# Optimization experiments

Measured on AMD Instinct MI355X. Metric: run time of the kernel, lower is better.

## Reference

```python
import jax, jax.numpy as jnp
import numpy as np

NQ = 4  # qubits
NL = 2  # layers actually used by the circuit body
BATCH = 1048576

def _c64(a):
    return a.astype(jnp.complex64)

def _ry(t):
    # RY(t) = [[cos(t/2), -sin(t/2)], [sin(t/2), cos(t/2)]]; t scalar or [B]
    c, s = jnp.cos(t / 2), jnp.sin(t / 2)
    return _c64(jnp.stack([jnp.stack([c, -s], -1), jnp.stack([s, c], -1)], -2))

def _rx(t):
    # RX(t) = [[cos(t/2), -i sin(t/2)], [-i sin(t/2), cos(t/2)]]
    c, s = _c64(jnp.cos(t / 2)), _c64(jnp.sin(t / 2))
    return jnp.stack([jnp.stack([c, -1j * s], -1), jnp.stack([-1j * s, c], -1)], -2)

def _rz(t):
    # RZ(t) = diag(exp(-i t/2), exp(i t/2))
    ph = _c64(t / 2)
    em, ep = jnp.exp(-1j * ph), jnp.exp(1j * ph)
    z = jnp.zeros_like(em)
    return jnp.stack([jnp.stack([em, z], -1), jnp.stack([z, ep], -1)], -2)

def _apply1q(state, gate, wire):
    # state: [B, 2,2,2,2]; gate: [2,2] (shared) or [B,2,2] (per-sample angle)
    s = jnp.moveaxis(state, wire + 1, -1)
    if gate.ndim == 3:
        out = jnp.einsum('b...j,bij->b...i', s, gate)
    else:
        out = jnp.einsum('b...j,ij->b...i', s, gate)
    return jnp.moveaxis(out, -1, wire + 1)

def _cnot(state, c, t):
    # bring control to axis 1, target to axis 2; flip target where control==1
    s = jnp.moveaxis(state, (c + 1, t + 1), (1, 2))
    s = jnp.stack([s[:, 0], jnp.flip(s[:, 1], axis=1)], axis=1)
    return jnp.moveaxis(s, (1, 2), (c + 1, t + 1))

def _circuit(x, weights):
    B = x.shape[0]
    state = jnp.zeros((B, 2 ** NQ), jnp.complex64).at[:, 0].set(1.0)
    state = state.reshape((B,) + (2,) * NQ)
    # angle encoding: RY(x_i) on wire i (per-sample angles)
    for i in range(NQ):
        state = _apply1q(state, _ry(x[:, i]), i)
    w = weights.reshape(NL, NQ, 3)
    for layer in range(NL):
        for i in range(NQ):
            state = _apply1q(state, _rx(w[layer, i, 0]), i)
            state = _apply1q(state, _ry(w[layer, i, 1]), i)
            state = _apply1q(state, _rz(w[layer, i, 2]), i)
        for i in range(NQ - 1):
            state = _cnot(state, i, i + 1)
        state = _cnot(state, NQ - 1, 0)
    # expval PauliZ on wire 0: +|amp|^2 for q0=0, -|amp|^2 for q0=1
    p = state.real ** 2 + state.imag ** 2
    p = p.reshape(B, 2, -1).sum(-1)
    return (p[:, 0] - p[:, 1]).astype(jnp.float32)

def setup_inputs() -> dict:
    key = jax.random.key(0)
    k1, k2 = jax.random.split(key)
    x = jax.random.normal(k1, (BATCH, NQ), jnp.float32)
    weights = jax.random.normal(k2, (NL * NQ * 3,), jnp.float32)
    return {"x": x, "weights": weights}

def reference(x, weights):
    return _circuit(x, weights)
```

## Files before the change

### kernel.cpp

```cpp
#include <hip/hip_runtime.h>
#include <hip/hip_bf16.h>


#define BLOCK 256
#define VEC 4

__global__ __launch_bounds__(BLOCK) void qnn_fused_kernel(
    const float4* __restrict__ x, const float* __restrict__ w,
    float* __restrict__ out, int n) {

    __shared__ float Ur[16][17], Ui[16][17];
    __shared__ float Msh[256];
    __shared__ float Ks[81];

    const int t = threadIdx.x;

    {
        const int j = t >> 4;
        const int k = t & 15;
        float ur = (k == j) ? 1.0f : 0.0f;
        float ui = 0.0f;

        #pragma unroll
        for (int layer = 0; layer < 2; ++layer) {
            #pragma unroll
            for (int q = 0; q < 4; ++q) {
                const int bit = 3 - q;
                const int str = 1 << bit;
                const int kb = (k >> bit) & 1;
                float c, s, pr, pi, nr, ni;
                __sincosf(w[(layer * 4 + q) * 3 + 0] * 0.5f, &s, &c);
                pr = __shfl_xor(ur, str);
                pi = __shfl_xor(ui, str);
                nr = c * ur + s * pi;
                ni = c * ui - s * pr;
                ur = nr; ui = ni;
                __sincosf(w[(layer * 4 + q) * 3 + 1] * 0.5f, &s, &c);
                pr = __shfl_xor(ur, str);
                pi = __shfl_xor(ui, str);
                {
                    const float sg = kb ? s : -s;
                    nr = c * ur + sg * pr;
                    ni = c * ui + sg * pi;
                }
                ur = nr; ui = ni;
                __sincosf(w[(layer * 4 + q) * 3 + 2] * 0.5f, &s, &c);
                {
                    const float sz = kb ? s : -s;
                    nr = c * ur - sz * ui;
                    ni = c * ui + sz * ur;
                }
                ur = nr; ui = ni;
            }
            #pragma unroll
            for (int g = 0; g < 4; ++g) {
                const int cw = g;
                const int tw = (g + 1) & 3;
                const int bc = 3 - cw, bt = 3 - tw;
                const float pr = __shfl_xor(ur, 1 << bt);
                const float pi = __shfl_xor(ui, 1 << bt);
                const bool ctl = (k >> bc) & 1;
                ur = ctl ? pr : ur;
                ui = ctl ? pi : ui;
            }
        }
        Ur[k][j] = ur;
        Ui[k][j] = ui;
    }
    __syncthreads();

    {
        const int a = t >> 4, b = t & 15;
        float acc = 0.0f;
        #pragma unroll
        for (int kk = 0; kk < 16; ++kk) {
            const float v2 = Ur[kk][a] * Ur[kk][b] + Ui[kk][a] * Ui[kk][b];
            acc += (kk & 8) ? -v2 : v2;
        }
        Msh[t] = acc;
    }
    __syncthreads();

    if (t < 81) {
        const int d0 = t / 27, d1 = (t / 9) % 3, d2 = (t / 3) % 3, d3 = t % 3;
        const int gd[4] = {d3, d2, d1, d0};
        float sum = 0.0f;
        #pragma unroll
        for (int m = 0; m < 16; ++m) {
            int a2 = 0, b2 = 0;
            float sign = 1.0f;
            #pragma unroll
            for (int p = 0; p < 4; ++p) {
                const int cp = (m >> p) & 1;
                if (gd[p] == 2) { a2 |= cp << p; b2 |= (1 - cp) << p; }
                else {
                    a2 |= cp << p; b2 |= cp << p;
                    if (gd[p] == 1 && cp) sign = -sign;
                }
            }
            sum += sign * Msh[a2 * 16 + b2];
        }
        Ks[t] = sum * 0.0625f;
    }
    __syncthreads();

    const int gid = blockIdx.x * BLOCK + t;
    const int stride = gridDim.x * BLOCK;

    for (int i0 = gid; i0 < n; i0 += stride * VEC) {
        int idx[VEC];
        bool ok[VEC];
        float4 xv[VEC];
        #pragma unroll
        for (int v = 0; v < VEC; ++v) {
            const int ii = i0 + v * stride;
            ok[v] = ii < n;
            idx[v] = ok[v] ? ii : (n - 1);
            xv[v] = x[idx[v]];
        }

        float C[VEC][4], S[VEC][4];
        #pragma unroll
        for (int v = 0; v < VEC; ++v) {
            __sincosf(xv[v].x, &S[v][0], &C[v][0]);
            __sincosf(xv[v].y, &S[v][1], &C[v][1]);
            __sincosf(xv[v].z, &S[v][2], &C[v][2]);
            __sincosf(xv[v].w, &S[v][3], &C[v][3]);
        }

        float r[VEC];
        #pragma unroll
        for (int d0 = 0; d0 < 3; ++d0) {
            float a1[VEC];
            #pragma unroll
            for (int d1 = 0; d1 < 3; ++d1) {
                float a2[VEC];
                #pragma unroll
                for (int d2 = 0; d2 < 3; ++d2) {
                    const int base = ((d0 * 3 + d1) * 3 + d2) * 3;
                    const float k0 = Ks[base], k1 = Ks[base + 1], k2 = Ks[base + 2];
                    #pragma unroll
                    for (int v = 0; v < VEC; ++v) {
                        const float tt = fmaf(k2, S[v][3], fmaf(k1, C[v][3], k0));
                        if (d2 == 0) a2[v] = tt;
                        else a2[v] = fmaf(tt, (d2 == 1) ? C[v][2] : S[v][2], a2[v]);
                    }
                }
                #pragma unroll
                for (int v = 0; v < VEC; ++v) {
                    if (d1 == 0) a1[v] = a2[v];
                    else a1[v] = fmaf(a2[v], (d1 == 1) ? C[v][1] : S[v][1], a1[v]);
                }
            }
            #pragma unroll
            for (int v = 0; v < VEC; ++v) {
                if (d0 == 0) r[v] = a1[v];
                else r[v] = fmaf(a1[v], (d0 == 1) ? C[v][0] : S[v][0], r[v]);
            }
        }

        #pragma unroll
        for (int v = 0; v < VEC; ++v)
            if (ok[v]) out[idx[v]] = r[v];
    }
}

extern "C" void kernel_launch(void* const* d_in, const int* in_sizes, int n_in,
                              void* d_out, int out_size, void* d_ws, size_t ws_size,
                              hipStream_t stream) {
    const float* x = (const float*)d_in[0];
    const float* w = (const float*)d_in[1];
    float* out = (float*)d_out;

    const int n = in_sizes[0] / 4;

    int grid = (n + BLOCK * VEC - 1) / (BLOCK * VEC);
    if (grid < 1) grid = 1;
    if (grid > 4096) grid = 4096;

    qnn_fused_kernel<<<grid, BLOCK, 0, stream>>>((const float4*)x, w, out, n);
}
```

Baseline: 69.87 us.

## Prefetch inputs before matrix setup, use hardware sin/cos, vectorize coefficient loads

Issues the first batch of x loads before the per-block unitary and coefficient precomputation, so global memory latency overlaps that setup work. Later iterations are software-pipelined by loading the next chunk before computing the current one. __sincosf is replaced with the raw amdgcn sin/cos instructions on angles pre-scaled by 1/(2π), which skips range reduction and may lose accuracy for large inputs. The 81 coefficients are padded into float4 slots so each LDS read fetches three coefficients at once.

Result: no change. 70.28 us (+0.6%).

```diff
diff --git a/kernel.cpp b/kernel.cpp
--- a/kernel.cpp
+++ b/kernel.cpp
@@ -4,6 +4,7 @@
 
 #define BLOCK 256
 #define VEC 4
+#define INV_2PI 0.15915494309189535f
 
 __global__ __launch_bounds__(BLOCK) void qnn_fused_kernel(
     const float4* __restrict__ x, const float* __restrict__ w,
@@ -11,9 +12,20 @@
 
     __shared__ float Ur[16][17], Ui[16][17];
     __shared__ float Msh[256];
-    __shared__ float Ks[81];
+    __shared__ float4 Ks4[27];
 
     const int t = threadIdx.x;
+    const int gid = blockIdx.x * BLOCK + t;
+    const int stride = gridDim.x * BLOCK;
+    const int step = stride * VEC;
+
+    int i0 = gid;
+    float4 xv[VEC];
+    #pragma unroll
+    for (int v = 0; v < VEC; ++v) {
+        const int ii = i0 + v * stride;
+        xv[v] = x[(ii < n) ? ii : (n > 0 ? n - 1 : 0)];
+    }
 
     {
         const int j = t >> 4;
@@ -100,32 +112,33 @@
             }
             sum += sign * Msh[a2 * 16 + b2];
         }
-        Ks[t] = sum * 0.0625f;
+        ((float*)Ks4)[(t / 3) * 4 + (t % 3)] = sum * 0.0625f;
     }
     __syncthreads();
 
-    const int gid = blockIdx.x * BLOCK + t;
-    const int stride = gridDim.x * BLOCK;
-
-    for (int i0 = gid; i0 < n; i0 += stride * VEC) {
-        int idx[VEC];
-        bool ok[VEC];
-        float4 xv[VEC];
+    for (; i0 < n;) {
+        float C[VEC][4], S[VEC][4];
         #pragma unroll
         for (int v = 0; v < VEC; ++v) {
-            const int ii = i0 + v * stride;
-            ok[v] = ii < n;
-            idx[v] = ok[v] ? ii : (n - 1);
-            xv[v] = x[idx[v]];
-        }
-
-        float C[VEC][4], S[VEC][4];
-        #pragma unroll
-        for (int v = 0; v < VEC; ++v) {
-            __sincosf(xv[v].x, &S[v][0], &C[v][0]);
-            __sincosf(xv[v].y, &S[v][1], &C[v][1]);
-            __sincosf(xv[v].z, &S[v][2], &C[v][2]);
-            __sincosf(xv[v].w, &S[v][3], &C[v][3]);
+            const float r0 = xv[v].x * INV_2PI;
+            const float r1 = xv[v].y * INV_2PI;
+            const float r2 = xv[v].z * INV_2PI;
+            const float r3 = xv[v].w * INV_2PI;
+            S[v][0] = __builtin_amdgcn_sinf(r0); C[v][0] = __builtin_amdgcn_cosf(r0);
+            S[v][1] = __builtin_amdgcn_sinf(r1); C[v][1] = __builtin_amdgcn_cosf(r1);
+            S[v][2] = __builtin_amdgcn_sinf(r2); C[v][2] = __builtin_amdgcn_cosf(r2);
+            S[v][3] = __builtin_amdgcn_sinf(r3); C[v][3] = __builtin_amdgcn_cosf(r3);
+        }
+
+        const int inext = i0 + step;
+        const bool more = inext < n;
+        float4 xn[VEC];
+        if (more) {
+            #pragma unroll
+            for (int v = 0; v < VEC; ++v) {
+                const int ii = inext + v * stride;
+                xn[v] = x[(ii < n) ? ii : (n - 1)];
+            }
         }
 
         float r[VEC];
@@ -137,11 +150,10 @@
                 float a2[VEC];
                 #pragma unroll
                 for (int d2 = 0; d2 < 3; ++d2) {
-                    const int base = ((d0 * 3 + d1) * 3 + d2) * 3;
-                    const float k0 = Ks[base], k1 = Ks[base + 1], k2 = Ks[base + 2];
+                    const float4 kf = Ks4[(d0 * 3 + d1) * 3 + d2];
                     #pragma unroll
                     for (int v = 0; v < VEC; ++v) {
-                        const float tt = fmaf(k2, S[v][3], fmaf(k1, C[v][3], k0));
+                        const float tt = fmaf(kf.z, S[v][3], fmaf(kf.y, C[v][3], kf.x));
                         if (d2 == 0) a2[v] = tt;
                         else a2[v] = fmaf(tt, (d2 == 1) ? C[v][2] : S[v][2], a2[v]);
                     }
@@ -160,8 +172,16 @@
         }
 
         #pragma unroll
-        for (int v = 0; v < VEC; ++v)
-            if (ok[v]) out[idx[v]] = r[v];
+        for (int v = 0; v < VEC; ++v) {
+            const int ii = i0 + v * stride;
+            if (ii < n) out[ii] = r[v];
+        }
+
+        i0 = inext;
+        if (more) {
+            #pragma unroll
+            for (int v = 0; v < VEC; ++v) xv[v] = xn[v];
+        }
     }
 }
 
```
